# Kernel tuning notes

Measured on AMD Instinct MI355X. Metric: run time of the kernel, lower is better.

## Reference

```python
import jax, jax.numpy as jnp
import numpy as np

N_NODES = 100000
N_EDGES = 3200000
N_FEAT = 512
N_HID = 16
N_CLS = 7


def setup_inputs() -> dict:
    key = jax.random.key(0)
    k0, k1, k2, k3 = jax.random.split(key, 4)
    x = jax.random.normal(k0, (N_NODES, N_FEAT), dtype=jnp.float32)
    edge_index = jax.random.randint(k1, (2, N_EDGES), 0, N_NODES, dtype=jnp.int64)
    W1 = jax.random.normal(k2, (N_FEAT, N_HID), dtype=jnp.float32) * (1.0 / np.sqrt(N_FEAT))
    b1 = jnp.zeros((N_HID,), dtype=jnp.float32)
    W2 = jax.random.normal(k3, (N_HID, N_CLS), dtype=jnp.float32) * (1.0 / np.sqrt(N_HID))
    b2 = jnp.zeros((N_CLS,), dtype=jnp.float32)
    return {"x": x, "edge_index": edge_index, "W1": W1, "b1": b1, "W2": W2, "b2": b2}


def _graph_conv(x, src, dst, W, b, n_nodes):
    # transform-then-aggregate: keeps the gathered edge tensor at hidden width
    h = x @ W                                      # [N, out]
    agg = jax.ops.segment_sum(h[src], dst, num_segments=n_nodes)  # [N, out]
    return agg + b


def reference(x, edge_index, W1, b1, W2, b2):
    src, dst = edge_index[0], edge_index[1]
    h = jax.nn.relu(_graph_conv(x, src, dst, W1, b1, N_NODES))
    # dropout is identity in eval mode
    out = _graph_conv(h, src, dst, W2, b2, N_NODES)
    return jax.nn.log_softmax(out, axis=1)
```

## Files before the change

kernel.cpp:

```cpp
#include <hip/hip_runtime.h>

#define NN 100000
#define NE 3200000
#define NF 512
#define NH 16
#define NC 7

__global__ __launch_bounds__(256) void gemm1_kernel(const float* __restrict__ x,
                                                    const float* __restrict__ W1,
                                                    float* __restrict__ h0) {
  const int lane = threadIdx.x & 63;
  const int wave = (blockIdx.x * blockDim.x + threadIdx.x) >> 6;
  const int nwaves = (gridDim.x * blockDim.x) >> 6;

  float w[8][NH];
#pragma unroll
  for (int i = 0; i < 4; ++i) {
#pragma unroll
    for (int j = 0; j < NH; ++j) {
      w[i][j]     = W1[(4 * lane + i) * NH + j];
      w[4 + i][j] = W1[(256 + 4 * lane + i) * NH + j];
    }
  }

  for (int row = wave; row < NN; row += nwaves) {
    const float4* xr = (const float4*)(x + (size_t)row * NF);
    float4 a0 = xr[lane];
    float4 a1 = xr[64 + lane];
    float a[8] = {a0.x, a0.y, a0.z, a0.w, a1.x, a1.y, a1.z, a1.w};

    float acc[NH];
#pragma unroll
    for (int j = 0; j < NH; ++j) acc[j] = 0.f;
#pragma unroll
    for (int i = 0; i < 8; ++i) {
#pragma unroll
      for (int j = 0; j < NH; ++j) acc[j] += a[i] * w[i][j];
    }

    float outv = 0.f;
#pragma unroll
    for (int j = 0; j < NH; ++j) {
      float v = acc[j];
      v += __shfl_xor(v, 1);
      v += __shfl_xor(v, 2);
      v += __shfl_xor(v, 4);
      v += __shfl_xor(v, 8);
      v += __shfl_xor(v, 16);
      v += __shfl_xor(v, 32);
      if (lane == j) outv = v;
    }
    if (lane < NH) h0[(size_t)row * NH + lane] = outv;
  }
}

__global__ __launch_bounds__(256) void scatter16_kernel(const int* __restrict__ ei,
                                                        const float* __restrict__ h0,
                                                        float* __restrict__ agg) {
  long long gid = (long long)blockIdx.x * blockDim.x + threadIdx.x;
  int e = (int)(gid >> 4);
  if (e >= NE) return;
  int j = (int)(gid & 15);
  int s = ei[e];
  int d = ei[NE + e];
  atomicAdd(&agg[(size_t)d * NH + j], h0[(size_t)s * NH + j]);
}

__global__ __launch_bounds__(256) void transform_kernel(const float* __restrict__ agg1,
                                                        const float* __restrict__ b1,
                                                        const float* __restrict__ W2,
                                                        float* __restrict__ p) {
  int n = blockIdx.x * blockDim.x + threadIdx.x;
  if (n >= NN) return;
  const float4* r = (const float4*)(agg1 + (size_t)n * NH);
  float4 v0 = r[0], v1 = r[1], v2 = r[2], v3 = r[3];
  float h[NH] = {v0.x, v0.y, v0.z, v0.w, v1.x, v1.y, v1.z, v1.w,
                 v2.x, v2.y, v2.z, v2.w, v3.x, v3.y, v3.z, v3.w};
#pragma unroll
  for (int k = 0; k < NH; ++k) h[k] = fmaxf(h[k] + b1[k], 0.f);

#pragma unroll
  for (int j = 0; j < NC; ++j) {
    float acc = 0.f;
#pragma unroll
    for (int k = 0; k < NH; ++k) acc += h[k] * W2[k * NC + j];
    p[(size_t)n * 8 + j] = acc;
  }
}

__global__ __launch_bounds__(256) void scatter7_kernel(const int* __restrict__ ei,
                                                       const float* __restrict__ p,
                                                       float* __restrict__ agg) {
  long long gid = (long long)blockIdx.x * blockDim.x + threadIdx.x;
  int e = (int)(gid >> 3);
  if (e >= NE) return;
  int j = (int)(gid & 7);
  if (j >= NC) return;
  int s = ei[e];
  int d = ei[NE + e];
  atomicAdd(&agg[(size_t)d * 8 + j], p[(size_t)s * 8 + j]);
}

__global__ __launch_bounds__(256) void lsm_kernel(const float* __restrict__ agg2,
                                                  const float* __restrict__ b2,
                                                  float* __restrict__ out) {
  int n = blockIdx.x * blockDim.x + threadIdx.x;
  if (n >= NN) return;
  float z[NC];
  float m = -1e30f;
#pragma unroll
  for (int j = 0; j < NC; ++j) {
    z[j] = agg2[(size_t)n * 8 + j] + b2[j];
    m = fmaxf(m, z[j]);
  }
  float s = 0.f;
#pragma unroll
  for (int j = 0; j < NC; ++j) s += __expf(z[j] - m);
  float l = __logf(s);
#pragma unroll
  for (int j = 0; j < NC; ++j) out[(size_t)n * NC + j] = z[j] - m - l;
}

extern "C" void kernel_launch(void* const* d_in, const int* in_sizes, int n_in,
                              void* d_out, int out_size, void* d_ws, size_t ws_size,
                              hipStream_t stream) {
  const float* x  = (const float*)d_in[0];
  const int*   ei = (const int*)d_in[1];
  const float* W1 = (const float*)d_in[2];
  const float* b1 = (const float*)d_in[3];
  const float* W2 = (const float*)d_in[4];
  const float* b2 = (const float*)d_in[5];
  float* out = (float*)d_out;

  float* bufA = (float*)d_ws;
  float* bufB = bufA + (size_t)NN * NH;

  hipMemsetAsync(bufB, 0, (size_t)NN * NH * sizeof(float), stream);
  gemm1_kernel<<<2048, 256, 0, stream>>>(x, W1, bufA);
  scatter16_kernel<<<(int)(((long long)NE * 16 + 255) / 256), 256, 0, stream>>>(ei, bufA, bufB);
  transform_kernel<<<(NN + 255) / 256, 256, 0, stream>>>(bufB, b1, W2, bufA);
  hipMemsetAsync(bufB, 0, (size_t)NN * 8 * sizeof(float), stream);
  scatter7_kernel<<<(int)(((long long)NE * 8 + 255) / 256), 256, 0, stream>>>(ei, bufA, bufB);
  lsm_kernel<<<(NN + 255) / 256, 256, 0, stream>>>(bufB, b2, out);
}
```

Measured before the change: 705.6 us.

## Replace atomic edge scatter with CSR build and per-node gather aggregation

```diff
diff --git a/kernel.cpp b/kernel.cpp
--- a/kernel.cpp
+++ b/kernel.cpp
@@ -5,6 +5,7 @@
 #define NF 512
 #define NH 16
 #define NC 7
+#define NPARTS ((NN + 255) / 256)
 
 __global__ __launch_bounds__(256) void gemm1_kernel(const float* __restrict__ x,
                                                     const float* __restrict__ W1,
@@ -52,6 +53,168 @@
     }
     if (lane < NH) h0[(size_t)row * NH + lane] = outv;
   }
+}
+
+__global__ __launch_bounds__(256) void hist_kernel(const int* __restrict__ ei,
+                                                   int* __restrict__ deg) {
+  int e = blockIdx.x * 256 + threadIdx.x;
+  if (e < NE) atomicAdd(&deg[ei[NE + e]], 1);
+}
+
+__global__ __launch_bounds__(256) void scan1_kernel(const int* __restrict__ deg,
+                                                    int* __restrict__ offs,
+                                                    int* __restrict__ part) {
+  __shared__ int sm[256];
+  int tid = threadIdx.x;
+  int i = blockIdx.x * 256 + tid;
+  int v = (i < NN) ? deg[i] : 0;
+  sm[tid] = v;
+  __syncthreads();
+  for (int off = 1; off < 256; off <<= 1) {
+    int t = (tid >= off) ? sm[tid - off] : 0;
+    __syncthreads();
+    sm[tid] += t;
+    __syncthreads();
+  }
+  if (i < NN) offs[i] = sm[tid] - v;
+  if (tid == 255) part[blockIdx.x] = sm[255];
+}
+
+__global__ __launch_bounds__(512) void scan2_kernel(int* __restrict__ part) {
+  __shared__ int sm[512];
+  int t = threadIdx.x;
+  int v = (t < NPARTS) ? part[t] : 0;
+  sm[t] = v;
+  __syncthreads();
+  for (int off = 1; off < 512; off <<= 1) {
+    int u = (t >= off) ? sm[t - off] : 0;
+    __syncthreads();
+    sm[t] += u;
+    __syncthreads();
+  }
+  if (t < NPARTS) part[t] = sm[t] - v;
+}
+
+__global__ __launch_bounds__(256) void scan3_kernel(int* __restrict__ offs,
+                                                    int* __restrict__ cur,
+                                                    const int* __restrict__ part) {
+  int i = blockIdx.x * 256 + threadIdx.x;
+  if (i < NN) {
+    int v = offs[i] + part[i >> 8];
+    offs[i] = v;
+    cur[i] = v;
+  }
+  if (i == 0) offs[NN] = NE;
+}
+
+__global__ __launch_bounds__(256) void fill_kernel(const int* __restrict__ ei,
+                                                   int* __restrict__ cur,
+                                                   int* __restrict__ srcs) {
+  int e = blockIdx.x * 256 + threadIdx.x;
+  if (e < NE) {
+    int s = ei[e];
+    int d = ei[NE + e];
+    int pos = atomicAdd(&cur[d], 1);
+    srcs[pos] = s;
+  }
+}
+
+__global__ __launch_bounds__(256) void agg16_kernel(const int* __restrict__ offs,
+                                                    const int* __restrict__ srcs,
+                                                    const float* __restrict__ h0,
+                                                    float* __restrict__ agg) {
+  const int lane = threadIdx.x & 63;
+  const int wave = (blockIdx.x * blockDim.x + threadIdx.x) >> 6;
+  const int nw = (gridDim.x * blockDim.x) >> 6;
+  const int col = lane & 15;
+  const int slot = lane >> 4;
+
+  for (int n = wave; n < NN; n += nw) {
+    int beg = offs[n], end = offs[n + 1];
+    float acc = 0.f;
+    int e = beg + slot;
+    for (; e + 4 < end; e += 8) {
+      int s0 = srcs[e];
+      int s1 = srcs[e + 4];
+      acc += h0[(size_t)s0 * NH + col];
+      acc += h0[(size_t)s1 * NH + col];
+    }
+    if (e < end) acc += h0[(size_t)srcs[e] * NH + col];
+    acc += __shfl_xor(acc, 16);
+    acc += __shfl_xor(acc, 32);
+    if (lane < NH) agg[(size_t)n * NH + lane] = acc;
+  }
+}
+
+__global__ __launch_bounds__(256) void transform_kernel(const float* __restrict__ agg1,
+                                                        const float* __restrict__ b1,
+                                                        const float* __restrict__ W2,
+                                                        float* __restrict__ p) {
+  int n = blockIdx.x * blockDim.x + threadIdx.x;
+  if (n >= NN) return;
+  const float4* r = (const float4*)(agg1 + (size_t)n * NH);
+  float4 v0 = r[0], v1 = r[1], v2 = r[2], v3 = r[3];
+  float h[NH] = {v0.x, v0.y, v0.z, v0.w, v1.x, v1.y, v1.z, v1.w,
+                 v2.x, v2.y, v2.z, v2.w, v3.x, v3.y, v3.z, v3.w};
+#pragma unroll
+  for (int k = 0; k < NH; ++k) h[k] = fmaxf(h[k] + b1[k], 0.f);
+
+#pragma unroll
+  for (int j = 0; j < NC; ++j) {
+    float acc = 0.f;
+#pragma unroll
+    for (int k = 0; k < NH; ++k) acc += h[k] * W2[k * NC + j];
+    p[(size_t)n * 8 + j] = acc;
+  }
+  p[(size_t)n * 8 + 7] = 0.f;
+}
+
+__global__ __launch_bounds__(256) void agg8_kernel(const int* __restrict__ offs,
+                                                   const int* __restrict__ srcs,
+                                                   const float* __restrict__ p,
+                                                   float* __restrict__ agg) {
+  const int lane = threadIdx.x & 63;
+  const int wave = (blockIdx.x * blockDim.x + threadIdx.x) >> 6;
+  const int nw = (gridDim.x * blockDim.x) >> 6;
+  const int col = lane & 7;
+  const int slot = lane >> 3;
+
+  for (int n = wave; n < NN; n += nw) {
+    int beg = offs[n], end = offs[n + 1];
+    float acc = 0.f;
+    int e = beg + slot;
+    for (; e + 8 < end; e += 16) {
+      int s0 = srcs[e];
+      int s1 = srcs[e + 8];
+      acc += p[(size_t)s0 * 8 + col];
+      acc += p[(size_t)s1 * 8 + col];
+    }
+    if (e < end) acc += p[(size_t)srcs[e] * 8 + col];
+    acc += __shfl_xor(acc, 8);
+    acc += __shfl_xor(acc, 16);
+    acc += __shfl_xor(acc, 32);
+    if (lane < 8) agg[(size_t)n * 8 + lane] = acc;
+  }
+}
+
+__global__ __launch_bounds__(256) void lsm_kernel(const float* __restrict__ agg2,
+                                                  const float* __restrict__ b2,
+                                                  float* __restrict__ out) {
+  int n = blockIdx.x * blockDim.x + threadIdx.x;
+  if (n >= NN) return;
+  float z[NC];
+  float m = -1e30f;
+#pragma unroll
+  for (int j = 0; j < NC; ++j) {
+    z[j] = agg2[(size_t)n * 8 + j] + b2[j];
+    m = fmaxf(m, z[j]);
+  }
+  float s = 0.f;
+#pragma unroll
+  for (int j = 0; j < NC; ++j) s += __expf(z[j] - m);
+  float l = __logf(s);
+#pragma unroll
+  for (int j = 0; j < NC; ++j) out[(size_t)n * NC + j] = z[j] - m - l;
 }
 
 __global__ __launch_bounds__(256) void scatter16_kernel(const int* __restrict__ ei,
@@ -64,28 +227,6 @@
   int s = ei[e];
   int d = ei[NE + e];
   atomicAdd(&agg[(size_t)d * NH + j], h0[(size_t)s * NH + j]);
-}
-
-__global__ __launch_bounds__(256) void transform_kernel(const float* __restrict__ agg1,
-                                                        const float* __restrict__ b1,
-                                                        const float* __restrict__ W2,
-                                                        float* __restrict__ p) {
-  int n = blockIdx.x * blockDim.x + threadIdx.x;
-  if (n >= NN) return;
-  const float4* r = (const float4*)(agg1 + (size_t)n * NH);
-  float4 v0 = r[0], v1 = r[1], v2 = r[2], v3 = r[3];
-  float h[NH] = {v0.x, v0.y, v0.z, v0.w, v1.x, v1.y, v1.z, v1.w,
-                 v2.x, v2.y, v2.z, v2.w, v3.x, v3.y, v3.z, v3.w};
-#pragma unroll
-  for (int k = 0; k < NH; ++k) h[k] = fmaxf(h[k] + b1[k], 0.f);
-
-#pragma unroll
-  for (int j = 0; j < NC; ++j) {
-    float acc = 0.f;
-#pragma unroll
-    for (int k = 0; k < NH; ++k) acc += h[k] * W2[k * NC + j];
-    p[(size_t)n * 8 + j] = acc;
-  }
 }
 
 __global__ __launch_bounds__(256) void scatter7_kernel(const int* __restrict__ ei,
@@ -101,26 +242,6 @@
   atomicAdd(&agg[(size_t)d * 8 + j], p[(size_t)s * 8 + j]);
 }
 
-__global__ __launch_bounds__(256) void lsm_kernel(const float* __restrict__ agg2,
-                                                  const float* __restrict__ b2,
-                                                  float* __restrict__ out) {
-  int n = blockIdx.x * blockDim.x + threadIdx.x;
-  if (n >= NN) return;
-  float z[NC];
-  float m = -1e30f;
-#pragma unroll
-  for (int j = 0; j < NC; ++j) {
-    z[j] = agg2[(size_t)n * 8 + j] + b2[j];
-    m = fmaxf(m, z[j]);
-  }
-  float s = 0.f;
-#pragma unroll
-  for (int j = 0; j < NC; ++j) s += __expf(z[j] - m);
-  float l = __logf(s);
-#pragma unroll
-  for (int j = 0; j < NC; ++j) out[(size_t)n * NC + j] = z[j] - m - l;
-}
-
 extern "C" void kernel_launch(void* const* d_in, const int* in_sizes, int n_in,
                               void* d_out, int out_size, void* d_ws, size_t ws_size,
                               hipStream_t stream) {
@@ -132,14 +253,37 @@
   const float* b2 = (const float*)d_in[5];
   float* out = (float*)d_out;
 
-  float* bufA = (float*)d_ws;
-  float* bufB = bufA + (size_t)NN * NH;
-
-  hipMemsetAsync(bufB, 0, (size_t)NN * NH * sizeof(float), stream);
-  gemm1_kernel<<<2048, 256, 0, stream>>>(x, W1, bufA);
-  scatter16_kernel<<<(int)(((long long)NE * 16 + 255) / 256), 256, 0, stream>>>(ei, bufA, bufB);
-  transform_kernel<<<(NN + 255) / 256, 256, 0, stream>>>(bufB, b1, W2, bufA);
-  hipMemsetAsync(bufB, 0, (size_t)NN * 8 * sizeof(float), stream);
-  scatter7_kernel<<<(int)(((long long)NE * 8 + 255) / 256), 256, 0, stream>>>(ei, bufA, bufB);
-  lsm_kernel<<<(NN + 255) / 256, 256, 0, stream>>>(bufB, b2, out);
-}
+  float* h0p  = (float*)d_ws;
+  float* aggp = h0p + (size_t)NN * NH;
+  int*   offs = (int*)(aggp + (size_t)NN * NH);
+  int*   cur  = offs + (NN + 1);
+  int*   part = cur + NN;
+  int*   srcs = part + 512;
+  size_t need = (size_t)((char*)(srcs + NE) - (char*)d_ws);
+
+  if (ws_size >= need) {
+    hipMemsetAsync(cur, 0, (size_t)NN * sizeof(int), stream);
+    hist_kernel<<<(NE + 255) / 256, 256, 0, stream>>>(ei, cur);
+    scan1_kernel<<<NPARTS, 256, 0, stream>>>(cur, offs, part);
+    scan2_kernel<<<1, 512, 0, stream>>>(part);
+    scan3_kernel<<<NPARTS, 256, 0, stream>>>(offs, cur, part);
+    fill_kernel<<<(NE + 255) / 256, 256, 0, stream>>>(ei, cur, srcs);
+
+    gemm1_kernel<<<2048, 256, 0, stream>>>(x, W1, h0p);
+    agg16_kernel<<<2048, 256, 0, stream>>>(offs, srcs, h0p, aggp);
+    transform_kernel<<<(NN + 255) / 256, 256, 0, stream>>>(aggp, b1, W2, h0p);
+    agg8_kernel<<<2048, 256, 0, stream>>>(offs, srcs, h0p, aggp);
+    lsm_kernel<<<(NN + 255) / 256, 256, 0, stream>>>(aggp, b2, out);
+  } else {
+    float* bufA = (float*)d_ws;
+    float* bufB = bufA + (size_t)NN * NH;
+
+    hipMemsetAsync(bufB, 0, (size_t)NN * NH * sizeof(float), stream);
+    gemm1_kernel<<<2048, 256, 0, stream>>>(x, W1, bufA);
+    scatter16_kernel<<<(int)(((long long)NE * 16 + 255) / 256), 256, 0, stream>>>(ei, bufA, bufB);
+    transform_kernel<<<(NN + 255) / 256, 256, 0, stream>>>(bufB, b1, W2, bufA);
+    hipMemsetAsync(bufB, 0, (size_t)NN * 8 * sizeof(float), stream);
+    scatter7_kernel<<<(int)(((long long)NE * 8 + 255) / 256), 256, 0, stream>>>(ei, bufA, bufB);
+    lsm_kernel<<<(NN + 255) / 256, 256, 0, stream>>>(bufB, b2, out);
+  }
+}
```

New measurement: 856.9 us. +21.4%, slower.

## Bucket edges by destination and aggregate in LDS instead of global atomics

Applied to the files above, without the earlier changes.

```diff
diff --git a/kernel.cpp b/kernel.cpp
--- a/kernel.cpp
+++ b/kernel.cpp
@@ -5,6 +5,11 @@
 #define NF 512
 #define NH 16
 #define NC 7
+
+#define NB   512
+#define SPAN 196
+#define NBLK 256
+#define EPB  (NE / NBLK)
 
 __global__ __launch_bounds__(256) void gemm1_kernel(const float* __restrict__ x,
                                                     const float* __restrict__ W1,
@@ -54,6 +59,164 @@
   }
 }
 
+__global__ __launch_bounds__(512) void countK(const int* __restrict__ ei,
+                                              int* __restrict__ bucketCount,
+                                              int* __restrict__ blockBase) {
+  __shared__ int cnt[NB];
+  const int b = blockIdx.x, tid = threadIdx.x;
+  cnt[tid] = 0;
+  __syncthreads();
+  const int base = b * EPB;
+  for (int e = tid; e < EPB; e += 512) {
+    int d = ei[NE + base + e];
+    atomicAdd(&cnt[d / SPAN], 1);
+  }
+  __syncthreads();
+  int c = cnt[tid];
+  blockBase[b * NB + tid] = c ? atomicAdd(&bucketCount[tid], c) : 0;
+}
+
+__global__ __launch_bounds__(512) void scanK(const int* __restrict__ bucketCount,
+                                             int* __restrict__ bucketOffs) {
+  __shared__ int sm[NB];
+  const int t = threadIdx.x;
+  int v = bucketCount[t];
+  sm[t] = v;
+  __syncthreads();
+  for (int off = 1; off < NB; off <<= 1) {
+    int u = (t >= off) ? sm[t - off] : 0;
+    __syncthreads();
+    sm[t] += u;
+    __syncthreads();
+  }
+  bucketOffs[t] = sm[t] - v;
+  if (t == NB - 1) bucketOffs[NB] = NE;
+}
+
+__global__ __launch_bounds__(512) void scatK(const int* __restrict__ ei,
+                                             const int* __restrict__ bucketOffs,
+                                             const int* __restrict__ blockBase,
+                                             unsigned* __restrict__ pairs) {
+  __shared__ int cur[NB];
+  const int b = blockIdx.x, tid = threadIdx.x;
+  cur[tid] = 0;
+  __syncthreads();
+  const int base = b * EPB;
+  for (int e = tid; e < EPB; e += 512) {
+    int s = ei[base + e];
+    int d = ei[NE + base + e];
+    int j = d / SPAN;
+    int dl = d - j * SPAN;
+    int r = atomicAdd(&cur[j], 1);
+    pairs[bucketOffs[j] + blockBase[b * NB + j] + r] = (unsigned)s | ((unsigned)dl << 17);
+  }
+}
+
+__global__ __launch_bounds__(512) void agg16K(const int* __restrict__ bucketOffs,
+                                              const unsigned* __restrict__ pairs,
+                                              const float* __restrict__ h0,
+                                              float* __restrict__ agg) {
+  __shared__ float acc[SPAN * NH];
+  const int j = blockIdx.x, tid = threadIdx.x;
+  for (int i = tid; i < SPAN * NH; i += 512) acc[i] = 0.f;
+  __syncthreads();
+  const int beg = bucketOffs[j], end = bucketOffs[j + 1];
+  const int col = tid & 15, slot = tid >> 4;
+  int e = beg + slot;
+  for (; e + 32 < end; e += 64) {
+    unsigned pk0 = pairs[e];
+    unsigned pk1 = pairs[e + 32];
+    float v0 = h0[(size_t)(pk0 & 0x1FFFF) * NH + col];
+    float v1 = h0[(size_t)(pk1 & 0x1FFFF) * NH + col];
+    atomicAdd(&acc[(pk0 >> 17) * NH + col], v0);
+    atomicAdd(&acc[(pk1 >> 17) * NH + col], v1);
+  }
+  if (e < end) {
+    unsigned pk = pairs[e];
+    atomicAdd(&acc[(pk >> 17) * NH + col], h0[(size_t)(pk & 0x1FFFF) * NH + col]);
+  }
+  __syncthreads();
+  const int lo = j * SPAN;
+  for (int i = tid; i < SPAN * NH; i += 512) {
+    int node = lo + (i >> 4);
+    if (node < NN) agg[(size_t)node * NH + (i & 15)] = acc[i];
+  }
+}
+
+__global__ __launch_bounds__(256) void transform_kernel(const float* __restrict__ agg1,
+                                                        const float* __restrict__ b1,
+                                                        const float* __restrict__ W2,
+                                                        float* __restrict__ p) {
+  int n = blockIdx.x * blockDim.x + threadIdx.x;
+  if (n >= NN) return;
+  const float4* r = (const float4*)(agg1 + (size_t)n * NH);
+  float4 v0 = r[0], v1 = r[1], v2 = r[2], v3 = r[3];
+  float h[NH] = {v0.x, v0.y, v0.z, v0.w, v1.x, v1.y, v1.z, v1.w,
+                 v2.x, v2.y, v2.z, v2.w, v3.x, v3.y, v3.z, v3.w};
+#pragma unroll
+  for (int k = 0; k < NH; ++k) h[k] = fmaxf(h[k] + b1[k], 0.f);
+
+#pragma unroll
+  for (int j = 0; j < NC; ++j) {
+    float acc = 0.f;
+#pragma unroll
+    for (int k = 0; k < NH; ++k) acc += h[k] * W2[k * NC + j];
+    p[(size_t)n * 8 + j] = acc;
+  }
+  p[(size_t)n * 8 + 7] = 0.f;
+}
+
+__global__ __launch_bounds__(512) void agg8K(const int* __restrict__ bucketOffs,
+                                             const unsigned* __restrict__ pairs,
+                                             const float* __restrict__ p,
+                                             float* __restrict__ agg) {
+  __shared__ float acc[SPAN * 8];
+  const int j = blockIdx.x, tid = threadIdx.x;
+  for (int i = tid; i < SPAN * 8; i += 512) acc[i] = 0.f;
+  __syncthreads();
+  const int beg = bucketOffs[j], end = bucketOffs[j + 1];
+  const int col = tid & 7, slot = tid >> 3;
+  int e = beg + slot;
+  for (; e + 64 < end; e += 128) {
+    unsigned pk0 = pairs[e];
+    unsigned pk1 = pairs[e + 64];
+    float v0 = p[(size_t)(pk0 & 0x1FFFF) * 8 + col];
+    float v1 = p[(size_t)(pk1 & 0x1FFFF) * 8 + col];
+    atomicAdd(&acc[(pk0 >> 17) * 8 + col], v0);
+    atomicAdd(&acc[(pk1 >> 17) * 8 + col], v1);
+  }
+  if (e < end) {
+    unsigned pk = pairs[e];
+    atomicAdd(&acc[(pk >> 17) * 8 + col], p[(size_t)(pk & 0x1FFFF) * 8 + col]);
+  }
+  __syncthreads();
+  const int lo = j * SPAN;
+  for (int i = tid; i < SPAN * 8; i += 512) {
+    int node = lo + (i >> 3);
+    if (node < NN) agg[(size_t)node * 8 + (i & 7)] = acc[i];
+  }
+}
+
+__global__ __launch_bounds__(256) void lsm_kernel(const float* __restrict__ agg2,
+                                                  const float* __restrict__ b2,
+                                                  float* __restrict__ out) {
+  int n = blockIdx.x * blockDim.x + threadIdx.x;
+  if (n >= NN) return;
+  float z[NC];
+  float m = -1e30f;
+#pragma unroll
+  for (int j = 0; j < NC; ++j) {
+    z[j] = agg2[(size_t)n * 8 + j] + b2[j];
+    m = fmaxf(m, z[j]);
+  }
+  float s = 0.f;
+#pragma unroll
+  for (int j = 0; j < NC; ++j) s += __expf(z[j] - m);
+  float l = __logf(s);
+#pragma unroll
+  for (int j = 0; j < NC; ++j) out[(size_t)n * NC + j] = z[j] - m - l;
+}
+
 __global__ __launch_bounds__(256) void scatter16_kernel(const int* __restrict__ ei,
                                                         const float* __restrict__ h0,
                                                         float* __restrict__ agg) {
@@ -64,28 +227,6 @@
   int s = ei[e];
   int d = ei[NE + e];
   atomicAdd(&agg[(size_t)d * NH + j], h0[(size_t)s * NH + j]);
-}
-
-__global__ __launch_bounds__(256) void transform_kernel(const float* __restrict__ agg1,
-                                                        const float* __restrict__ b1,
-                                                        const float* __restrict__ W2,
-                                                        float* __restrict__ p) {
-  int n = blockIdx.x * blockDim.x + threadIdx.x;
-  if (n >= NN) return;
-  const float4* r = (const float4*)(agg1 + (size_t)n * NH);
-  float4 v0 = r[0], v1 = r[1], v2 = r[2], v3 = r[3];
-  float h[NH] = {v0.x, v0.y, v0.z, v0.w, v1.x, v1.y, v1.z, v1.w,
-                 v2.x, v2.y, v2.z, v2.w, v3.x, v3.y, v3.z, v3.w};
-#pragma unroll
-  for (int k = 0; k < NH; ++k) h[k] = fmaxf(h[k] + b1[k], 0.f);
-
-#pragma unroll
-  for (int j = 0; j < NC; ++j) {
-    float acc = 0.f;
-#pragma unroll
-    for (int k = 0; k < NH; ++k) acc += h[k] * W2[k * NC + j];
-    p[(size_t)n * 8 + j] = acc;
-  }
 }
 
 __global__ __launch_bounds__(256) void scatter7_kernel(const int* __restrict__ ei,
@@ -101,26 +242,6 @@
   atomicAdd(&agg[(size_t)d * 8 + j], p[(size_t)s * 8 + j]);
 }
 
-__global__ __launch_bounds__(256) void lsm_kernel(const float* __restrict__ agg2,
-                                                  const float* __restrict__ b2,
-                                                  float* __restrict__ out) {
-  int n = blockIdx.x * blockDim.x + threadIdx.x;
-  if (n >= NN) return;
-  float z[NC];
-  float m = -1e30f;
-#pragma unroll
-  for (int j = 0; j < NC; ++j) {
-    z[j] = agg2[(size_t)n * 8 + j] + b2[j];
-    m = fmaxf(m, z[j]);
-  }
-  float s = 0.f;
-#pragma unroll
-  for (int j = 0; j < NC; ++j) s += __expf(z[j] - m);
-  float l = __logf(s);
-#pragma unroll
-  for (int j = 0; j < NC; ++j) out[(size_t)n * NC + j] = z[j] - m - l;
-}
-
 extern "C" void kernel_launch(void* const* d_in, const int* in_sizes, int n_in,
                               void* d_out, int out_size, void* d_ws, size_t ws_size,
                               hipStream_t stream) {
@@ -132,14 +253,35 @@
   const float* b2 = (const float*)d_in[5];
   float* out = (float*)d_out;
 
-  float* bufA = (float*)d_ws;
-  float* bufB = bufA + (size_t)NN * NH;
-
-  hipMemsetAsync(bufB, 0, (size_t)NN * NH * sizeof(float), stream);
-  gemm1_kernel<<<2048, 256, 0, stream>>>(x, W1, bufA);
-  scatter16_kernel<<<(int)(((long long)NE * 16 + 255) / 256), 256, 0, stream>>>(ei, bufA, bufB);
-  transform_kernel<<<(NN + 255) / 256, 256, 0, stream>>>(bufB, b1, W2, bufA);
-  hipMemsetAsync(bufB, 0, (size_t)NN * 8 * sizeof(float), stream);
-  scatter7_kernel<<<(int)(((long long)NE * 8 + 255) / 256), 256, 0, stream>>>(ei, bufA, bufB);
-  lsm_kernel<<<(NN + 255) / 256, 256, 0, stream>>>(bufB, b2, out);
-}
+  float*    h0p  = (float*)d_ws;
+  float*    aggp = h0p + (size_t)NN * NH;
+  unsigned* pairs = (unsigned*)(aggp + (size_t)NN * NH);
+  int* bucketCount = (int*)(pairs + NE);
+  int* bucketOffs  = bucketCount + NB;
+  int* blockBase   = (int*)aggp;
+  size_t need = (size_t)((char*)(bucketOffs + NB + 1) - (char*)d_ws);
+
+  if (ws_size >= need) {
+    hipMemsetAsync(bucketCount, 0, NB * sizeof(int), stream);
+    countK<<<NBLK, 512, 0, stream>>>(ei, bucketCount, blockBase);
+    scanK<<<1, NB, 0, stream>>>(bucketCount, bucketOffs);
+    scatK<<<NBLK, 512, 0, stream>>>(ei, bucketOffs, blockBase, pairs);
+
+    gemm1_kernel<<<2048, 256, 0, stream>>>(x, W1, h0p);
+    agg16K<<<NB, 512, 0, stream>>>(bucketOffs, pairs, h0p, aggp);
+    transform_kernel<<<(NN + 255) / 256, 256, 0, stream>>>(aggp, b1, W2, h0p);
+    agg8K<<<NB, 512, 0, stream>>>(bucketOffs, pairs, h0p, aggp);
+    lsm_kernel<<<(NN + 255) / 256, 256, 0, stream>>>(aggp, b2, out);
+  } else {
+    float* bufA = (float*)d_ws;
+    float* bufB = bufA + (size_t)NN * NH;
+
+    hipMemsetAsync(bufB, 0, (size_t)NN * NH * sizeof(float), stream);
+    gemm1_kernel<<<2048, 256, 0, stream>>>(x, W1, bufA);
+    scatter16_kernel<<<(int)(((long long)NE * 16 + 255) / 256), 256, 0, stream>>>(ei, bufA, bufB);
+    transform_kernel<<<(NN + 255) / 256, 256, 0, stream>>>(bufB, b1, W2, bufA);
+    hipMemsetAsync(bufB, 0, (size_t)NN * 8 * sizeof(float), stream);
+    scatter7_kernel<<<(int)(((long long)NE * 8 + 255) / 256), 256, 0, stream>>>(ei, bufA, bufB);
+    lsm_kernel<<<(NN + 255) / 256, 256, 0, stream>>>(bufB, b2, out);
+  }
+}
```

Result: slower. 832.2 us (+17.9%).
